# Kernel optimization log

Measured on AMD Instinct MI355X. Metric: run time of the kernel, lower is better.

Reference implementation:

```python
import jax, jax.numpy as jnp
import numpy as np

NUM_HEADS = 16
NUM_KV_HEADS = 4
HEAD_DIM = 128
LAYER_IDX = 5
MASK_VALUE = -65504.0  # torch.finfo(torch.float16).min


def setup_inputs() -> dict:
    key = jax.random.key(0)
    ks = jax.random.split(key, 7)
    B, S, H = 2, 2048, 2048
    hidden_states = jax.random.normal(ks[0], (B, S, H), dtype=jnp.float32)
    k = jax.random.normal(ks[1], (B, NUM_KV_HEADS, S, HEAD_DIM), dtype=jnp.float32)
    v = jax.random.normal(ks[2], (B, NUM_KV_HEADS, S, HEAD_DIM), dtype=jnp.float32)
    std = 0.02
    w_q = jax.random.normal(ks[3], (H, H), dtype=jnp.float32) * std
    b_q = jnp.zeros((H,), dtype=jnp.float32)
    w_proj = jax.random.normal(ks[4], (H, H), dtype=jnp.float32) * (std / np.sqrt(2 * 24))
    b_proj = jnp.zeros((H,), dtype=jnp.float32)
    return {"hidden_states": hidden_states, "key": k, "value": v,
            "w_q": w_q, "b_q": b_q, "w_proj": w_proj, "b_proj": b_proj}


def reference(hidden_states, key, value, w_q, b_q, w_proj, b_proj):
    B, S, H = hidden_states.shape
    G = NUM_HEADS // NUM_KV_HEADS  # query heads per kv head
    dtype = hidden_states.dtype

    # query projection -> [B, kv_heads, group, S, head_dim]
    q = hidden_states @ w_q.T + b_q
    q = q.reshape(B, S, NUM_KV_HEADS, G, HEAD_DIM).transpose(0, 2, 3, 1, 4)

    # bigcode-style fp32 softmax with layer-wise unscale
    unscale = float(LAYER_IDX + 1)  # scale_attention_softmax_in_fp32 and upcast
    scale_factor = (1.0 / unscale) * (HEAD_DIM ** -0.5)  # scale_attn_weights

    # scores: [B, kv_heads, group, S_q, S_k]
    scores = jnp.einsum('bkgsd,bktd->bkgst', q, key) * scale_factor

    causal = jnp.tril(jnp.ones((S, S), dtype=bool))  # [S_q, S_k]
    scores = jnp.where(causal, scores, jnp.asarray(MASK_VALUE, dtype=scores.dtype))

    probs = jax.nn.softmax((scores * unscale).astype(jnp.float32), axis=-1).astype(dtype)

    out = jnp.einsum('bkgst,bktd->bkgsd', probs, value)
    out = out.transpose(0, 3, 1, 2, 4).reshape(B, S, H)
    out = out @ w_proj.T + b_proj
    return out
```

## Files before the change

kernel.cpp:

```cpp
#include <hip/hip_runtime.h>
#include <math.h>


#define RSQ128 0.08838834764831845
#define LOG2E  1.4426950408889634
#define RS2L   ((float)(RSQ128 * LOG2E))
#define MASK2  (-567000.0f)
#define CAP2   24.0f

typedef __attribute__((ext_vector_type(8))) short short8;
typedef __attribute__((ext_vector_type(4))) float f32x4;
typedef __attribute__((ext_vector_type(16))) float f32x16;

static __device__ __forceinline__ unsigned short f2bf(float x) {
    union { float f; unsigned u; } v; v.f = x;
    unsigned r = v.u + 0x7FFFu + ((v.u >> 16) & 1u);
    return (unsigned short)(r >> 16);
}

static __device__ __forceinline__ unsigned pack_bf16(float lo, float hi) {
#if __has_builtin(__builtin_amdgcn_cvt_pk_bf16_f32)
    return __builtin_bit_cast(unsigned, __builtin_amdgcn_cvt_pk_bf16_f32(lo, hi));
#else
    return (unsigned)f2bf(lo) | ((unsigned)f2bf(hi) << 16);
#endif
}

static __device__ __forceinline__ float fexp2(float x) {
#if __has_builtin(__builtin_amdgcn_exp2f)
    return __builtin_amdgcn_exp2f(x);
#else
    return exp2f(x);
#endif
}

static __device__ __forceinline__ void gl_lds16(const void* g, void* l) {
    __builtin_amdgcn_global_load_lds(
        (const __attribute__((address_space(1))) void*)g,
        (__attribute__((address_space(3))) void*)l, 16, 0, 0);
}

__global__ void cvt_bf16(const float* __restrict__ in, unsigned short* __restrict__ out) {
    const int i = (blockIdx.x * 256 + threadIdx.x) * 8;
    const float4 a = *(const float4*)(in + i);
    const float4 b = *(const float4*)(in + i + 4);
    short8 o;
    o[0] = (short)f2bf(a.x); o[1] = (short)f2bf(a.y);
    o[2] = (short)f2bf(a.z); o[3] = (short)f2bf(a.w);
    o[4] = (short)f2bf(b.x); o[5] = (short)f2bf(b.y);
    o[6] = (short)f2bf(b.z); o[7] = (short)f2bf(b.w);
    *(short8*)(out + i) = o;
}

__global__ void kprep_bf16(const float* __restrict__ K, unsigned short* __restrict__ Kpk) {
    const int t = blockIdx.x, bkh = blockIdx.y, tid = threadIdx.x;
    const float* src = K + ((size_t)bkh * 2048 + t * 32) * 128;
    unsigned short* dst = Kpk + ((size_t)bkh * 64 + t) * 4096;
#pragma unroll
    for (int p = 0; p < 2; ++p) {
        const int g = p * 256 + tid;
        const int ch = g >> 5, key = g & 31;
        const float4 a = *(const float4*)(src + key * 128 + ch * 8);
        const float4 b = *(const float4*)(src + key * 128 + ch * 8 + 4);
        short8 o;
        o[0] = (short)f2bf(a.x); o[1] = (short)f2bf(a.y);
        o[2] = (short)f2bf(a.z); o[3] = (short)f2bf(a.w);
        o[4] = (short)f2bf(b.x); o[5] = (short)f2bf(b.y);
        o[6] = (short)f2bf(b.z); o[7] = (short)f2bf(b.w);
        *(short8*)(dst + ch * 256 + key * 8) = o;
    }
}

__global__ void vprep_bf16(const float* __restrict__ V, unsigned short* __restrict__ Vpk) {
    __shared__ float Ts[32][132];
    const int t = blockIdx.x, bkh = blockIdx.y, tid = threadIdx.x;
    const float* src = V + ((size_t)bkh * 2048 + t * 32) * 128;
    unsigned short* dst = Vpk + ((size_t)bkh * 64 + t) * 4096;
#pragma unroll
    for (int p = 0; p < 4; ++p) {
        const int g = p * 256 + tid;
        const int key = g >> 5, cq = g & 31;
        const float4 v = *(const float4*)(src + key * 128 + cq * 4);
        *(float4*)&Ts[key][cq * 4] = v;
    }
    __syncthreads();
#pragma unroll
    for (int p = 0; p < 2; ++p) {
        const int g = p * 256 + tid;
        const int kc = g >> 7, d = g & 127;
        short8 o;
#pragma unroll
        for (int j = 0; j < 8; ++j) o[j] = (short)f2bf(Ts[kc * 8 + j][d]);
        *(short8*)(dst + kc * 1024 + d * 8) = o;
    }
}

template <bool BF16OUT>
__global__ __launch_bounds__(512, 2) void gemm_nt_sk(
    const unsigned short* __restrict__ A,
    const unsigned short* __restrict__ W,
    const float* __restrict__ bias,
    void* __restrict__ Cout, int M, int N, int K, float oscale)
{
    __shared__ __align__(16) unsigned short SMEM[32768];
    unsigned short* Asb = SMEM;
    unsigned short* Wsb = SMEM + 16384;

    const int tid = threadIdx.x;
    const int g = tid >> 8;
    const int t2 = tid & 255;
    const int lane = tid & 63;
    const int wq = (tid >> 6) & 3;
    const int wm = wq & 1, wn = wq >> 1;
    const int m0 = blockIdx.y * 128, n0 = blockIdx.x * 128;
    const int r0 = t2 >> 2, c0 = t2 & 3;
    const int Kh = K >> 1;

    const unsigned short* Ag = A + (size_t)(m0 + r0) * K + g * Kh + c0 * 8;
    const unsigned short* Wg = W + (size_t)(n0 + r0) * K + g * Kh + c0 * 8;

    f32x4 acc[4][4];
#pragma unroll
    for (int i = 0; i < 4; ++i)
#pragma unroll
        for (int j = 0; j < 4; ++j) acc[i][j] = (f32x4){0.f, 0.f, 0.f, 0.f};

    const int lm = lane & 15, lk = (lane >> 4) * 8;
    unsigned short* As0 = Asb + g * 8192;
    unsigned short* Ws0 = Wsb + g * 8192;

    gl_lds16(Ag,                  As0 + t2 * 8);
    gl_lds16(Ag + (size_t)64 * K, As0 + (t2 + 256) * 8);
    gl_lds16(Wg,                  Ws0 + t2 * 8);
    gl_lds16(Wg + (size_t)64 * K, Ws0 + (t2 + 256) * 8);

    int buf = 0;
    for (int k0 = 0; k0 < Kh; k0 += 32) {
        __syncthreads();
        const int kn = k0 + 32;
        if (kn < Kh) {
            unsigned short* Ad = As0 + (buf ^ 1) * 4096;
            unsigned short* Wd = Ws0 + (buf ^ 1) * 4096;
            gl_lds16(Ag + kn,                  Ad + t2 * 8);
            gl_lds16(Ag + (size_t)64 * K + kn, Ad + (t2 + 256) * 8);
            gl_lds16(Wg + kn,                  Wd + t2 * 8);
            gl_lds16(Wg + (size_t)64 * K + kn, Wd + (t2 + 256) * 8);
        }

        const unsigned short* Ar = As0 + buf * 4096;
        const unsigned short* Wr = Ws0 + buf * 4096;
        short8 a[4], b[4];
#pragma unroll
        for (int i = 0; i < 4; ++i)
            a[i] = *(const short8*)&Ar[(64 * wm + 16 * i + lm) * 32 + lk];
#pragma unroll
        for (int j = 0; j < 4; ++j)
            b[j] = *(const short8*)&Wr[(64 * wn + 16 * j + lm) * 32 + lk];
#pragma unroll
        for (int i = 0; i < 4; ++i)
#pragma unroll
            for (int j = 0; j < 4; ++j)
                acc[i][j] = __builtin_amdgcn_mfma_f32_16x16x32_bf16(a[i], b[j], acc[i][j], 0, 0, 0);
        buf ^= 1;
    }

    float* MRG = (float*)SMEM;
    __syncthreads();
    if (g == 1) {
#pragma unroll
        for (int i = 0; i < 4; ++i)
#pragma unroll
            for (int j = 0; j < 4; ++j) {
                float4 v4;
                v4.x = acc[i][j][0]; v4.y = acc[i][j][1];
                v4.z = acc[i][j][2]; v4.w = acc[i][j][3];
                *(float4*)&MRG[((i * 4 + j) * 256 + wq * 64 + lane) * 4] = v4;
            }
    }
    __syncthreads();
    if (g == 0) {
        float bv[4];
#pragma unroll
        for (int j = 0; j < 4; ++j) bv[j] = bias[n0 + 64 * wn + 16 * j + lm];
#pragma unroll
        for (int i = 0; i < 4; ++i)
#pragma unroll
            for (int j = 0; j < 4; ++j) {
                const float4 v4 = *(const float4*)&MRG[((i * 4 + j) * 256 + wq * 64 + lane) * 4];
                const float s[4] = {v4.x, v4.y, v4.z, v4.w};
#pragma unroll
                for (int reg = 0; reg < 4; ++reg) {
                    const int row = m0 + 64 * wm + 16 * i + 4 * (lane >> 4) + reg;
                    const int col = n0 + 64 * wn + 16 * j + lm;
                    const float v = (acc[i][j][reg] + s[reg] + bv[j]) * oscale;
                    if (BF16OUT) ((unsigned short*)Cout)[(size_t)row * N + col] = f2bf(v);
                    else         ((float*)Cout)[(size_t)row * N + col] = v;
                }
            }
    }
}

__global__ __launch_bounds__(256, 4) void attn_mfma7(
    const unsigned short* __restrict__ Q,
    const unsigned short* __restrict__ Kpk,
    const unsigned short* __restrict__ Vpk,
    unsigned short* __restrict__ O)
{
    __shared__ __align__(16) unsigned short Ks[2][4096];
    __shared__ __align__(16) unsigned short Vs[2][4096];
    __shared__ float Lsm[2][64];

    const int tid = threadIdx.x, lane = tid & 63, w = tid >> 6;
    const int qhalf = w & 1, pz = w >> 1;
    const int h2 = lane >> 5, ln = lane & 31;

    const int bid = blockIdx.x;
    const int jj = bid >> 5;
    const int aa = jj & 7, bb = jj >> 3;
    const int qb = 8 * bb + ((bb & 1) ? (7 - aa) : aa);
    const int bh = bid & 31;
    const int s0 = qb * 64;
    const int b = bh >> 4, h = bh & 15, kh = h >> 2;

    const unsigned short* Kbase = Kpk + (size_t)(b * 4 + kh) * 64 * 4096;
    const unsigned short* Vbase = Vpk + (size_t)(b * 4 + kh) * 64 * 4096;

    const unsigned short* stsrc = (pz == 0 ? Kbase : Vbase) + (size_t)qhalf * 4096 + lane * 8;
    unsigned short* stdst = (pz == 0 ? Ks[qhalf] : Vs[qhalf]);

    const int qg = s0 + 32 * qhalf + ln;
    const unsigned short* Qp = Q + (size_t)(b * 2048 + qg) * 2048 + h * 128 + h2 * 8;
    short8 Qreg[8];
#pragma unroll
    for (int ks = 0; ks < 8; ++ks) Qreg[ks] = *(const short8*)(Qp + ks * 16);

    f32x16 Ot[4];
#pragma unroll
    for (int mt = 0; mt < 4; ++mt)
#pragma unroll
        for (int r = 0; r < 16; ++r) Ot[mt][r] = 0.f;
    float l_ = 0.f;

    const int wq_hi = s0 + 32 * qhalf + 31;
    const int myofs = 32 * pz;

    for (int j = 0; j <= qb; ++j) {
        __syncthreads();
        {
            const unsigned short* sp = stsrc + (size_t)j * 8192;
#pragma unroll
            for (int i = 0; i < 8; ++i)
                gl_lds16(sp + i * 512, stdst + i * 512);
        }
        __syncthreads();

        const int t0 = 64 * j + myofs;
        if (t0 <= wq_hi) {
            const unsigned short* KsA = Ks[pz] + h2 * 256 + ln * 8;
            const unsigned short* VsA = Vs[pz] + h2 * 1024 + ln * 8;

            f32x16 St;
#pragma unroll
            for (int r = 0; r < 16; ++r) St[r] = 0.f;
#pragma unroll
            for (int ks = 0; ks < 8; ++ks) {
                const short8 a = *(const short8*)(KsA + ks * 512);
                St = __builtin_amdgcn_mfma_f32_32x32x16_bf16(a, Qreg[ks], St, 0, 0, 0);
            }

            float s_loc = 0.f;
            unsigned Pp[8];
            if (t0 + 31 <= s0 + 32 * qhalf) {
#pragma unroll
                for (int p = 0; p < 8; ++p) {
                    const float p0 = fexp2(St[2 * p] - CAP2);
                    const float p1 = fexp2(St[2 * p + 1] - CAP2);
                    s_loc += p0 + p1;
                    Pp[p] = pack_bf16(p0, p1);
                }
            } else {
#pragma unroll
                for (int p = 0; p < 8; ++p) {
                    const int k0 = t0 + (2 * p & 3) + 8 * (2 * p >> 2) + 4 * h2;
                    const int k1 = t0 + ((2 * p + 1) & 3) + 8 * ((2 * p + 1) >> 2) + 4 * h2;
                    const float p0 = (k0 <= qg) ? fexp2(St[2 * p] - CAP2) : 0.f;
                    const float p1 = (k1 <= qg) ? fexp2(St[2 * p + 1] - CAP2) : 0.f;
                    s_loc += p0 + p1;
                    Pp[p] = pack_bf16(p0, p1);
                }
            }
            s_loc += __shfl_xor(s_loc, 32);
            l_ += s_loc;

#pragma unroll
            for (int ks4 = 0; ks4 < 2; ++ks4) {
                const unsigned pa = Pp[4 * ks4 + 0], pb = Pp[4 * ks4 + 1];
                const unsigned pc = Pp[4 * ks4 + 2], pd = Pp[4 * ks4 + 3];
                const unsigned x0 = (unsigned)__shfl_xor((int)(h2 ? pa : pc), 32);
                const unsigned x1 = (unsigned)__shfl_xor((int)(h2 ? pb : pd), 32);
                union { unsigned u[4]; short8 s8; } fr;
                fr.u[0] = h2 ? x0 : pa;
                fr.u[1] = h2 ? x1 : pb;
                fr.u[2] = h2 ? pc : x0;
                fr.u[3] = h2 ? pd : x1;
#pragma unroll
                for (int mt = 0; mt < 4; ++mt) {
                    const short8 a = *(const short8*)(VsA + ks4 * 2048 + mt * 256);
                    Ot[mt] = __builtin_amdgcn_mfma_f32_32x32x16_bf16(a, fr.s8, Ot[mt], 0, 0, 0);
                }
            }
        }
    }

    __syncthreads();
    if (pz == 1) {
        float* dst = qhalf ? (float*)Vs : (float*)Ks;
#pragma unroll
        for (int mt = 0; mt < 4; ++mt)
#pragma unroll
            for (int g = 0; g < 4; ++g) {
                float4 v4;
                v4.x = Ot[mt][4 * g + 0]; v4.y = Ot[mt][4 * g + 1];
                v4.z = Ot[mt][4 * g + 2]; v4.w = Ot[mt][4 * g + 3];
                *(float4*)&dst[lane * 64 + (((mt * 4 + g + lane) & 15) * 4)] = v4;
            }
        Lsm[qhalf][lane] = l_;
    }
    __syncthreads();
    if (pz == 0) {
        const float* src = qhalf ? (const float*)Vs : (const float*)Ks;
        l_ += Lsm[qhalf][lane];
#pragma unroll
        for (int mt = 0; mt < 4; ++mt)
#pragma unroll
            for (int g = 0; g < 4; ++g) {
                const float4 v4 = *(const float4*)&src[lane * 64 + (((mt * 4 + g + lane) & 15) * 4)];
                Ot[mt][4 * g + 0] += v4.x;
                Ot[mt][4 * g + 1] += v4.y;
                Ot[mt][4 * g + 2] += v4.z;
                Ot[mt][4 * g + 3] += v4.w;
            }
    }
    __syncthreads();

    if (pz == 0) {
        unsigned short* Es = (unsigned short*)Ks + qhalf * 4096;
        const float inv = 1.0f / l_;
#pragma unroll
        for (int mt = 0; mt < 4; ++mt)
#pragma unroll
            for (int g = 0; g < 4; ++g) {
                uint2 pk;
                pk.x = pack_bf16(Ot[mt][4 * g + 0] * inv, Ot[mt][4 * g + 1] * inv);
                pk.y = pack_bf16(Ot[mt][4 * g + 2] * inv, Ot[mt][4 * g + 3] * inv);
                const int chunk = (4 * mt + g) ^ (ln & 15);
                *(uint2*)&Es[ln * 128 + chunk * 8 + 4 * h2] = pk;
            }
    }
    __syncthreads();
    if (pz == 0) {
        unsigned short* Es = (unsigned short*)Ks + qhalf * 4096;
#pragma unroll
        for (int pp = 0; pp < 8; ++pp) {
            const int f = pp * 64 + lane;
            const int q = f >> 4, c = f & 15;
            const short8 v = *(const short8*)&Es[q * 128 + ((c ^ (q & 15)) * 8)];
            *(short8*)(O + (size_t)(b * 2048 + s0 + 32 * qhalf + q) * 2048 + h * 128 + c * 8) = v;
        }
    }
}

extern "C" void kernel_launch(void* const* d_in, const int* in_sizes, int n_in,
                              void* d_out, int out_size, void* d_ws, size_t ws_size,
                              hipStream_t stream) {
    const float* hs = (const float*)d_in[0];
    const float* k  = (const float*)d_in[1];
    const float* v  = (const float*)d_in[2];
    const float* wq = (const float*)d_in[3];
    const float* bq = (const float*)d_in[4];
    const float* wp = (const float*)d_in[5];
    const float* bp = (const float*)d_in[6];
    float* out = (float*)d_out;

    unsigned short* hsb  = (unsigned short*)d_ws;
    unsigned short* wqb  = hsb  + 8388608;
    unsigned short* kpk  = wqb  + 4194304;
    unsigned short* vpk  = kpk  + 2097152;
    unsigned short* qbuf = vpk  + 2097152;
    unsigned short* abuf = qbuf + 8388608;
    unsigned short* wpb  = hsb;

    cvt_bf16<<<4096, 256, 0, stream>>>(hs, hsb);
    cvt_bf16<<<2048, 256, 0, stream>>>(wq, wqb);
    kprep_bf16<<<dim3(64, 8), 256, 0, stream>>>(k, kpk);
    vprep_bf16<<<dim3(64, 8), 256, 0, stream>>>(v, vpk);

    dim3 gG(16, 32);
    gemm_nt_sk<true><<<gG, 512, 0, stream>>>(hsb, wqb, bq, qbuf, 4096, 2048, 2048, RS2L);
    cvt_bf16<<<2048, 256, 0, stream>>>(wp, wpb);
    attn_mfma7<<<1024, 256, 0, stream>>>(qbuf, kpk, vpk, abuf);
    gemm_nt_sk<false><<<gG, 512, 0, stream>>>(abuf, wpb, bp, out, 4096, 2048, 2048, 1.0f);
}
```

Measured before the change: 298.9 us.

## Pair causal query blocks per workgroup and double-buffer K/V LDS loads

The attention kernel now processes two query blocks per workgroup (qb and 31-qb), so each workgroup does an equal amount of causal work and the grid halves to 512 blocks. K/V tiles are double-buffered in LDS, with the next tile's global-to-LDS copy issued before computing on the current one and explicit vmcnt waits. Block indexing is reordered so neighbouring blocks share a kv head. LDS use doubles and launch bounds drop to 2 waves per EU, which lowers occupancy in exchange for overlapping loads with compute.

```diff
diff --git a/kernel.cpp b/kernel.cpp
--- a/kernel.cpp
+++ b/kernel.cpp
@@ -200,14 +200,14 @@
     }
 }
 
-__global__ __launch_bounds__(256, 4) void attn_mfma7(
+__global__ __launch_bounds__(256, 2) void attn_mfma8(
     const unsigned short* __restrict__ Q,
     const unsigned short* __restrict__ Kpk,
     const unsigned short* __restrict__ Vpk,
     unsigned short* __restrict__ O)
 {
-    __shared__ __align__(16) unsigned short Ks[2][4096];
-    __shared__ __align__(16) unsigned short Vs[2][4096];
+    __shared__ __align__(16) unsigned short Ks[2][2][4096];
+    __shared__ __align__(16) unsigned short Vs[2][2][4096];
     __shared__ float Lsm[2][64];
 
     const int tid = threadIdx.x, lane = tid & 63, w = tid >> 6;
@@ -215,157 +215,176 @@
     const int h2 = lane >> 5, ln = lane & 31;
 
     const int bid = blockIdx.x;
-    const int jj = bid >> 5;
-    const int aa = jj & 7, bb = jj >> 3;
-    const int qb = 8 * bb + ((bb & 1) ? (7 - aa) : aa);
-    const int bh = bid & 31;
-    const int s0 = qb * 64;
-    const int b = bh >> 4, h = bh & 15, kh = h >> 2;
+    const int grp = bid & 7;
+    const int idx = bid >> 3;
+    const int b = grp >> 2, kh = grp & 3;
+    const int pr = idx >> 2, hl = idx & 3;
+    const int h = kh * 4 + hl;
 
     const unsigned short* Kbase = Kpk + (size_t)(b * 4 + kh) * 64 * 4096;
     const unsigned short* Vbase = Vpk + (size_t)(b * 4 + kh) * 64 * 4096;
-
     const unsigned short* stsrc = (pz == 0 ? Kbase : Vbase) + (size_t)qhalf * 4096 + lane * 8;
-    unsigned short* stdst = (pz == 0 ? Ks[qhalf] : Vs[qhalf]);
-
-    const int qg = s0 + 32 * qhalf + ln;
-    const unsigned short* Qp = Q + (size_t)(b * 2048 + qg) * 2048 + h * 128 + h2 * 8;
-    short8 Qreg[8];
-#pragma unroll
-    for (int ks = 0; ks < 8; ++ks) Qreg[ks] = *(const short8*)(Qp + ks * 16);
-
-    f32x16 Ot[4];
-#pragma unroll
-    for (int mt = 0; mt < 4; ++mt)
-#pragma unroll
-        for (int r = 0; r < 16; ++r) Ot[mt][r] = 0.f;
-    float l_ = 0.f;
-
-    const int wq_hi = s0 + 32 * qhalf + 31;
     const int myofs = 32 * pz;
 
-    for (int j = 0; j <= qb; ++j) {
-        __syncthreads();
+    for (int ph = 0; ph < 2; ++ph) {
+        const int qb = ph ? pr : 31 - pr;
+        const int s0 = qb * 64;
+        const int qg = s0 + 32 * qhalf + ln;
+        const int wq_hi = s0 + 32 * qhalf + 31;
+
+        const unsigned short* Qp = Q + (size_t)(b * 2048 + qg) * 2048 + h * 128 + h2 * 8;
+        short8 Qreg[8];
+#pragma unroll
+        for (int ks = 0; ks < 8; ++ks) Qreg[ks] = *(const short8*)(Qp + ks * 16);
+
+        f32x16 Ot[4];
+#pragma unroll
+        for (int mt = 0; mt < 4; ++mt)
+#pragma unroll
+            for (int r = 0; r < 16; ++r) Ot[mt][r] = 0.f;
+        float l_ = 0.f;
+
+        __syncthreads();
+
         {
-            const unsigned short* sp = stsrc + (size_t)j * 8192;
+            unsigned short* sd = (pz == 0) ? &Ks[0][qhalf][0] : &Vs[0][qhalf][0];
 #pragma unroll
             for (int i = 0; i < 8; ++i)
-                gl_lds16(sp + i * 512, stdst + i * 512);
-        }
-        __syncthreads();
-
-        const int t0 = 64 * j + myofs;
-        if (t0 <= wq_hi) {
-            const unsigned short* KsA = Ks[pz] + h2 * 256 + ln * 8;
-            const unsigned short* VsA = Vs[pz] + h2 * 1024 + ln * 8;
-
-            f32x16 St;
-#pragma unroll
-            for (int r = 0; r < 16; ++r) St[r] = 0.f;
-#pragma unroll
-            for (int ks = 0; ks < 8; ++ks) {
-                const short8 a = *(const short8*)(KsA + ks * 512);
-                St = __builtin_amdgcn_mfma_f32_32x32x16_bf16(a, Qreg[ks], St, 0, 0, 0);
+                gl_lds16(stsrc + i * 512, sd + i * 512);
+        }
+
+        for (int j = 0; j <= qb; ++j) {
+            const int buf = j & 1;
+            if (j < qb) {
+                const unsigned short* sp = stsrc + (size_t)(j + 1) * 8192;
+                unsigned short* sd = (pz == 0) ? &Ks[buf ^ 1][qhalf][0] : &Vs[buf ^ 1][qhalf][0];
+#pragma unroll
+                for (int i = 0; i < 8; ++i)
+                    gl_lds16(sp + i * 512, sd + i * 512);
+                asm volatile("s_waitcnt vmcnt(8)" ::: "memory");
+            } else {
+                asm volatile("s_waitcnt vmcnt(0)" ::: "memory");
             }
-
-            float s_loc = 0.f;
-            unsigned Pp[8];
-            if (t0 + 31 <= s0 + 32 * qhalf) {
-#pragma unroll
-                for (int p = 0; p < 8; ++p) {
-                    const float p0 = fexp2(St[2 * p] - CAP2);
-                    const float p1 = fexp2(St[2 * p + 1] - CAP2);
-                    s_loc += p0 + p1;
-                    Pp[p] = pack_bf16(p0, p1);
-                }
-            } else {
-#pragma unroll
-                for (int p = 0; p < 8; ++p) {
-                    const int k0 = t0 + (2 * p & 3) + 8 * (2 * p >> 2) + 4 * h2;
-                    const int k1 = t0 + ((2 * p + 1) & 3) + 8 * ((2 * p + 1) >> 2) + 4 * h2;
-                    const float p0 = (k0 <= qg) ? fexp2(St[2 * p] - CAP2) : 0.f;
-                    const float p1 = (k1 <= qg) ? fexp2(St[2 * p + 1] - CAP2) : 0.f;
-                    s_loc += p0 + p1;
-                    Pp[p] = pack_bf16(p0, p1);
+            __builtin_amdgcn_s_barrier();
+            __builtin_amdgcn_sched_barrier(0);
+
+            const int t0 = 64 * j + myofs;
+            if (t0 <= wq_hi) {
+                const unsigned short* KsA = &Ks[buf][pz][0] + h2 * 256 + ln * 8;
+                const unsigned short* VsA = &Vs[buf][pz][0] + h2 * 1024 + ln * 8;
+
+                f32x16 St;
+#pragma unroll
+                for (int r = 0; r < 16; ++r) St[r] = 0.f;
+#pragma unroll
+                for (int ks = 0; ks < 8; ++ks) {
+                    const short8 a = *(const short8*)(KsA + ks * 512);
+                    St = __builtin_amdgcn_mfma_f32_32x32x16_bf16(a, Qreg[ks], St, 0, 0, 0);
+                }
+
+                float s_loc = 0.f;
+                unsigned Pp[8];
+                if (t0 + 31 <= s0 + 32 * qhalf) {
+#pragma unroll
+                    for (int p = 0; p < 8; ++p) {
+                        const float p0 = fexp2(St[2 * p] - CAP2);
+                        const float p1 = fexp2(St[2 * p + 1] - CAP2);
+                        s_loc += p0 + p1;
+                        Pp[p] = pack_bf16(p0, p1);
+                    }
+                } else {
+#pragma unroll
+                    for (int p = 0; p < 8; ++p) {
+                        const int k0 = t0 + (2 * p & 3) + 8 * (2 * p >> 2) + 4 * h2;
+                        const int k1 = t0 + ((2 * p + 1) & 3) + 8 * ((2 * p + 1) >> 2) + 4 * h2;
+                        const float p0 = (k0 <= qg) ? fexp2(St[2 * p] - CAP2) : 0.f;
+                        const float p1 = (k1 <= qg) ? fexp2(St[2 * p + 1] - CAP2) : 0.f;
+                        s_loc += p0 + p1;
+                        Pp[p] = pack_bf16(p0, p1);
+                    }
+                }
+                s_loc += __shfl_xor(s_loc, 32);
+                l_ += s_loc;
+
+#pragma unroll
+                for (int ks4 = 0; ks4 < 2; ++ks4) {
+                    const unsigned pa = Pp[4 * ks4 + 0], pb = Pp[4 * ks4 + 1];
+                    const unsigned pc = Pp[4 * ks4 + 2], pd = Pp[4 * ks4 + 3];
+                    const unsigned x0 = (unsigned)__shfl_xor((int)(h2 ? pa : pc), 32);
+                    const unsigned x1 = (unsigned)__shfl_xor((int)(h2 ? pb : pd), 32);
+                    union { unsigned u[4]; short8 s8; } fr;
+                    fr.u[0] = h2 ? x0 : pa;
+                    fr.u[1] = h2 ? x1 : pb;
+                    fr.u[2] = h2 ? pc : x0;
+                    fr.u[3] = h2 ? pd : x1;
+#pragma unroll
+                    for (int mt = 0; mt < 4; ++mt) {
+                        const short8 a = *(const short8*)(VsA + ks4 * 2048 + mt * 256);
+                        Ot[mt] = __builtin_amdgcn_mfma_f32_32x32x16_bf16(a, fr.s8, Ot[mt], 0, 0, 0);
+                    }
                 }
             }
-            s_loc += __shfl_xor(s_loc, 32);
-            l_ += s_loc;
-
-#pragma unroll
-            for (int ks4 = 0; ks4 < 2; ++ks4) {
-                const unsigned pa = Pp[4 * ks4 + 0], pb = Pp[4 * ks4 + 1];
-                const unsigned pc = Pp[4 * ks4 + 2], pd = Pp[4 * ks4 + 3];
-                const unsigned x0 = (unsigned)__shfl_xor((int)(h2 ? pa : pc), 32);
-                const unsigned x1 = (unsigned)__shfl_xor((int)(h2 ? pb : pd), 32);
-                union { unsigned u[4]; short8 s8; } fr;
-                fr.u[0] = h2 ? x0 : pa;
-                fr.u[1] = h2 ? x1 : pb;
-                fr.u[2] = h2 ? pc : x0;
-                fr.u[3] = h2 ? pd : x1;
-#pragma unroll
-                for (int mt = 0; mt < 4; ++mt) {
-                    const short8 a = *(const short8*)(VsA + ks4 * 2048 + mt * 256);
-                    Ot[mt] = __builtin_amdgcn_mfma_f32_32x32x16_bf16(a, fr.s8, Ot[mt], 0, 0, 0);
-                }
+
+            __builtin_amdgcn_sched_barrier(0);
+            __builtin_amdgcn_s_barrier();
+            __builtin_amdgcn_sched_barrier(0);
+        }
+
+        __syncthreads();
+        if (pz == 1) {
+            float* dst = qhalf ? (float*)Vs : (float*)Ks;
+#pragma unroll
+            for (int mt = 0; mt < 4; ++mt)
+#pragma unroll
+                for (int g = 0; g < 4; ++g) {
+                    float4 v4;
+                    v4.x = Ot[mt][4 * g + 0]; v4.y = Ot[mt][4 * g + 1];
+                    v4.z = Ot[mt][4 * g + 2]; v4.w = Ot[mt][4 * g + 3];
+                    *(float4*)&dst[lane * 64 + (((mt * 4 + g + lane) & 15) * 4)] = v4;
+                }
+            Lsm[qhalf][lane] = l_;
+        }
+        __syncthreads();
+        if (pz == 0) {
+            const float* src = qhalf ? (const float*)Vs : (const float*)Ks;
+            l_ += Lsm[qhalf][lane];
+#pragma unroll
+            for (int mt = 0; mt < 4; ++mt)
+#pragma unroll
+                for (int g = 0; g < 4; ++g) {
+                    const float4 v4 = *(const float4*)&src[lane * 64 + (((mt * 4 + g + lane) & 15) * 4)];
+                    Ot[mt][4 * g + 0] += v4.x;
+                    Ot[mt][4 * g + 1] += v4.y;
+                    Ot[mt][4 * g + 2] += v4.z;
+                    Ot[mt][4 * g + 3] += v4.w;
+                }
+        }
+        __syncthreads();
+
+        if (pz == 0) {
+            unsigned short* Es = (unsigned short*)Ks + qhalf * 4096;
+            const float inv = 1.0f / l_;
+#pragma unroll
+            for (int mt = 0; mt < 4; ++mt)
+#pragma unroll
+                for (int g = 0; g < 4; ++g) {
+                    uint2 pk;
+                    pk.x = pack_bf16(Ot[mt][4 * g + 0] * inv, Ot[mt][4 * g + 1] * inv);
+                    pk.y = pack_bf16(Ot[mt][4 * g + 2] * inv, Ot[mt][4 * g + 3] * inv);
+                    const int chunk = (4 * mt + g) ^ (ln & 15);
+                    *(uint2*)&Es[ln * 128 + chunk * 8 + 4 * h2] = pk;
+                }
+        }
+        __syncthreads();
+        if (pz == 0) {
+            unsigned short* Es = (unsigned short*)Ks + qhalf * 4096;
+#pragma unroll
+            for (int pp = 0; pp < 8; ++pp) {
+                const int f = pp * 64 + lane;
+                const int q = f >> 4, c = f & 15;
+                const short8 v = *(const short8*)&Es[q * 128 + ((c ^ (q & 15)) * 8)];
+                *(short8*)(O + (size_t)(b * 2048 + s0 + 32 * qhalf + q) * 2048 + h * 128 + c * 8) = v;
             }
-        }
-    }
-
-    __syncthreads();
-    if (pz == 1) {
-        float* dst = qhalf ? (float*)Vs : (float*)Ks;
-#pragma unroll
-        for (int mt = 0; mt < 4; ++mt)
-#pragma unroll
-            for (int g = 0; g < 4; ++g) {
-                float4 v4;
-                v4.x = Ot[mt][4 * g + 0]; v4.y = Ot[mt][4 * g + 1];
-                v4.z = Ot[mt][4 * g + 2]; v4.w = Ot[mt][4 * g + 3];
-                *(float4*)&dst[lane * 64 + (((mt * 4 + g + lane) & 15) * 4)] = v4;
-            }
-        Lsm[qhalf][lane] = l_;
-    }
-    __syncthreads();
-    if (pz == 0) {
-        const float* src = qhalf ? (const float*)Vs : (const float*)Ks;
-        l_ += Lsm[qhalf][lane];
-#pragma unroll
-        for (int mt = 0; mt < 4; ++mt)
-#pragma unroll
-            for (int g = 0; g < 4; ++g) {
-                const float4 v4 = *(const float4*)&src[lane * 64 + (((mt * 4 + g + lane) & 15) * 4)];
-                Ot[mt][4 * g + 0] += v4.x;
-                Ot[mt][4 * g + 1] += v4.y;
-                Ot[mt][4 * g + 2] += v4.z;
-                Ot[mt][4 * g + 3] += v4.w;
-            }
-    }
-    __syncthreads();
-
-    if (pz == 0) {
-        unsigned short* Es = (unsigned short*)Ks + qhalf * 4096;
-        const float inv = 1.0f / l_;
-#pragma unroll
-        for (int mt = 0; mt < 4; ++mt)
-#pragma unroll
-            for (int g = 0; g < 4; ++g) {
-                uint2 pk;
-                pk.x = pack_bf16(Ot[mt][4 * g + 0] * inv, Ot[mt][4 * g + 1] * inv);
-                pk.y = pack_bf16(Ot[mt][4 * g + 2] * inv, Ot[mt][4 * g + 3] * inv);
-                const int chunk = (4 * mt + g) ^ (ln & 15);
-                *(uint2*)&Es[ln * 128 + chunk * 8 + 4 * h2] = pk;
-            }
-    }
-    __syncthreads();
-    if (pz == 0) {
-        unsigned short* Es = (unsigned short*)Ks + qhalf * 4096;
-#pragma unroll
-        for (int pp = 0; pp < 8; ++pp) {
-            const int f = pp * 64 + lane;
-            const int q = f >> 4, c = f & 15;
-            const short8 v = *(const short8*)&Es[q * 128 + ((c ^ (q & 15)) * 8)];
-            *(short8*)(O + (size_t)(b * 2048 + s0 + 32 * qhalf + q) * 2048 + h * 128 + c * 8) = v;
         }
     }
 }
@@ -398,6 +417,6 @@
     dim3 gG(16, 32);
     gemm_nt_sk<true><<<gG, 512, 0, stream>>>(hsb, wqb, bq, qbuf, 4096, 2048, 2048, RS2L);
     cvt_bf16<<<2048, 256, 0, stream>>>(wp, wpb);
-    attn_mfma7<<<1024, 256, 0, stream>>>(qbuf, kpk, vpk, abuf);
+    attn_mfma8<<<512, 256, 0, stream>>>(qbuf, kpk, vpk, abuf);
     gemm_nt_sk<false><<<gG, 512, 0, stream>>>(abuf, wpb, bp, out, 4096, 2048, 2048, 1.0f);
 }
```

Result: faster. 273.6 us (-8.5%).

## Pair causal q-blocks per block and load K/V fragments directly into registers

Applied to the files above, without the earlier changes.

The attention kernel now launches 512 blocks, and each block handles two q-blocks (pr and 31-pr) in turn, which balances causal work across blocks. The LDS staging of K/V tiles and the per-iteration __syncthreads are removed. Each wave loads its K and V MFMA fragments straight from global memory into registers, relying on L2 reuse across the heads that share a KV head, which the new block ordering groups together. Launch bounds drop to 2 waves per EU to leave room for the larger register set. The risk is that global loads are no longer overlapped with compute and that occupancy is lower.

```diff
diff --git a/kernel.cpp b/kernel.cpp
--- a/kernel.cpp
+++ b/kernel.cpp
@@ -5,7 +5,6 @@
 #define RSQ128 0.08838834764831845
 #define LOG2E  1.4426950408889634
 #define RS2L   ((float)(RSQ128 * LOG2E))
-#define MASK2  (-567000.0f)
 #define CAP2   24.0f
 
 typedef __attribute__((ext_vector_type(8))) short short8;
@@ -200,14 +199,13 @@
     }
 }
 
-__global__ __launch_bounds__(256, 4) void attn_mfma7(
+__global__ __launch_bounds__(256, 2) void attn_mfma9(
     const unsigned short* __restrict__ Q,
     const unsigned short* __restrict__ Kpk,
     const unsigned short* __restrict__ Vpk,
     unsigned short* __restrict__ O)
 {
-    __shared__ __align__(16) unsigned short Ks[2][4096];
-    __shared__ __align__(16) unsigned short Vs[2][4096];
+    __shared__ __align__(16) float MRG[2][4096];
     __shared__ float Lsm[2][64];
 
     const int tid = threadIdx.x, lane = tid & 63, w = tid >> 6;
@@ -215,58 +213,59 @@
     const int h2 = lane >> 5, ln = lane & 31;
 
     const int bid = blockIdx.x;
-    const int jj = bid >> 5;
-    const int aa = jj & 7, bb = jj >> 3;
-    const int qb = 8 * bb + ((bb & 1) ? (7 - aa) : aa);
-    const int bh = bid & 31;
-    const int s0 = qb * 64;
-    const int b = bh >> 4, h = bh & 15, kh = h >> 2;
+    const int grp = bid & 7;
+    const int idx = bid >> 3;
+    const int b = grp >> 2, kh = grp & 3;
+    const int pr = idx >> 2, hl = idx & 3;
+    const int h = kh * 4 + hl;
 
     const unsigned short* Kbase = Kpk + (size_t)(b * 4 + kh) * 64 * 4096;
     const unsigned short* Vbase = Vpk + (size_t)(b * 4 + kh) * 64 * 4096;
-
-    const unsigned short* stsrc = (pz == 0 ? Kbase : Vbase) + (size_t)qhalf * 4096 + lane * 8;
-    unsigned short* stdst = (pz == 0 ? Ks[qhalf] : Vs[qhalf]);
-
-    const int qg = s0 + 32 * qhalf + ln;
-    const unsigned short* Qp = Q + (size_t)(b * 2048 + qg) * 2048 + h * 128 + h2 * 8;
-    short8 Qreg[8];
-#pragma unroll
-    for (int ks = 0; ks < 8; ++ks) Qreg[ks] = *(const short8*)(Qp + ks * 16);
-
-    f32x16 Ot[4];
-#pragma unroll
-    for (int mt = 0; mt < 4; ++mt)
-#pragma unroll
-        for (int r = 0; r < 16; ++r) Ot[mt][r] = 0.f;
-    float l_ = 0.f;
-
-    const int wq_hi = s0 + 32 * qhalf + 31;
+    const int koff = h2 * 256 + ln * 8;
+    const int voff = h2 * 1024 + ln * 8;
     const int myofs = 32 * pz;
 
-    for (int j = 0; j <= qb; ++j) {
-        __syncthreads();
-        {
-            const unsigned short* sp = stsrc + (size_t)j * 8192;
+    for (int ph = 0; ph < 2; ++ph) {
+        const int qb = ph ? pr : 31 - pr;
+        const int s0 = qb * 64;
+        const int qg = s0 + 32 * qhalf + ln;
+        const int wq_hi = s0 + 32 * qhalf + 31;
+
+        const unsigned short* Qp = Q + (size_t)(b * 2048 + qg) * 2048 + h * 128 + h2 * 8;
+        short8 Qreg[8];
+#pragma unroll
+        for (int ks = 0; ks < 8; ++ks) Qreg[ks] = *(const short8*)(Qp + ks * 16);
+
+        f32x16 Ot[4];
+#pragma unroll
+        for (int mt = 0; mt < 4; ++mt)
+#pragma unroll
+            for (int r = 0; r < 16; ++r) Ot[mt][r] = 0.f;
+        float l_ = 0.f;
+
+        __syncthreads();
+
+        for (int j = 0; j <= qb; ++j) {
+            const int t0 = 64 * j + myofs;
+            if (t0 > wq_hi) continue;
+
+            const unsigned short* Kt = Kbase + (size_t)(2 * j + pz) * 4096;
+            const unsigned short* Vt = Vbase + (size_t)(2 * j + pz) * 4096;
+
+            short8 kf[8], vf[8];
+#pragma unroll
+            for (int ks = 0; ks < 8; ++ks)
+                kf[ks] = *(const short8*)(Kt + ks * 512 + koff);
 #pragma unroll
             for (int i = 0; i < 8; ++i)
-                gl_lds16(sp + i * 512, stdst + i * 512);
-        }
-        __syncthreads();
-
-        const int t0 = 64 * j + myofs;
-        if (t0 <= wq_hi) {
-            const unsigned short* KsA = Ks[pz] + h2 * 256 + ln * 8;
-            const unsigned short* VsA = Vs[pz] + h2 * 1024 + ln * 8;
+                vf[i] = *(const short8*)(Vt + (i >> 2) * 2048 + (i & 3) * 256 + voff);
 
             f32x16 St;
 #pragma unroll
             for (int r = 0; r < 16; ++r) St[r] = 0.f;
 #pragma unroll
-            for (int ks = 0; ks < 8; ++ks) {
-                const short8 a = *(const short8*)(KsA + ks * 512);
-                St = __builtin_amdgcn_mfma_f32_32x32x16_bf16(a, Qreg[ks], St, 0, 0, 0);
-            }
+            for (int ks = 0; ks < 8; ++ks)
+                St = __builtin_amdgcn_mfma_f32_32x32x16_bf16(kf[ks], Qreg[ks], St, 0, 0, 0);
 
             float s_loc = 0.f;
             unsigned Pp[8];
@@ -304,68 +303,66 @@
                 fr.u[2] = h2 ? pc : x0;
                 fr.u[3] = h2 ? pd : x1;
 #pragma unroll
-                for (int mt = 0; mt < 4; ++mt) {
-                    const short8 a = *(const short8*)(VsA + ks4 * 2048 + mt * 256);
-                    Ot[mt] = __builtin_amdgcn_mfma_f32_32x32x16_bf16(a, fr.s8, Ot[mt], 0, 0, 0);
-                }
+                for (int mt = 0; mt < 4; ++mt)
+                    Ot[mt] = __builtin_amdgcn_mfma_f32_32x32x16_bf16(vf[ks4 * 4 + mt], fr.s8, Ot[mt], 0, 0, 0);
             }
         }
-    }
-
-    __syncthreads();
-    if (pz == 1) {
-        float* dst = qhalf ? (float*)Vs : (float*)Ks;
-#pragma unroll
-        for (int mt = 0; mt < 4; ++mt)
-#pragma unroll
-            for (int g = 0; g < 4; ++g) {
-                float4 v4;
-                v4.x = Ot[mt][4 * g + 0]; v4.y = Ot[mt][4 * g + 1];
-                v4.z = Ot[mt][4 * g + 2]; v4.w = Ot[mt][4 * g + 3];
-                *(float4*)&dst[lane * 64 + (((mt * 4 + g + lane) & 15) * 4)] = v4;
+
+        __syncthreads();
+        if (pz == 1) {
+            float* dst = MRG[qhalf];
+#pragma unroll
+            for (int mt = 0; mt < 4; ++mt)
+#pragma unroll
+                for (int g = 0; g < 4; ++g) {
+                    float4 v4;
+                    v4.x = Ot[mt][4 * g + 0]; v4.y = Ot[mt][4 * g + 1];
+                    v4.z = Ot[mt][4 * g + 2]; v4.w = Ot[mt][4 * g + 3];
+                    *(float4*)&dst[lane * 64 + (((mt * 4 + g + lane) & 15) * 4)] = v4;
+                }
+            Lsm[qhalf][lane] = l_;
+        }
+        __syncthreads();
+        if (pz == 0) {
+            const float* src = MRG[qhalf];
+            l_ += Lsm[qhalf][lane];
+#pragma unroll
+            for (int mt = 0; mt < 4; ++mt)
+#pragma unroll
+                for (int g = 0; g < 4; ++g) {
+                    const float4 v4 = *(const float4*)&src[lane * 64 + (((mt * 4 + g + lane) & 15) * 4)];
+                    Ot[mt][4 * g + 0] += v4.x;
+                    Ot[mt][4 * g + 1] += v4.y;
+                    Ot[mt][4 * g + 2] += v4.z;
+                    Ot[mt][4 * g + 3] += v4.w;
+                }
+        }
+        __syncthreads();
+
+        if (pz == 0) {
+            unsigned short* Es = (unsigned short*)MRG[qhalf];
+            const float inv = 1.0f / l_;
+#pragma unroll
+            for (int mt = 0; mt < 4; ++mt)
+#pragma unroll
+                for (int g = 0; g < 4; ++g) {
+                    uint2 pk;
+                    pk.x = pack_bf16(Ot[mt][4 * g + 0] * inv, Ot[mt][4 * g + 1] * inv);
+                    pk.y = pack_bf16(Ot[mt][4 * g + 2] * inv, Ot[mt][4 * g + 3] * inv);
+                    const int chunk = (4 * mt + g) ^ (ln & 15);
+                    *(uint2*)&Es[ln * 128 + chunk * 8 + 4 * h2] = pk;
+                }
+        }
+        __syncthreads();
+        if (pz == 0) {
+            unsigned short* Es = (unsigned short*)MRG[qhalf];
+#pragma unroll
+            for (int pp = 0; pp < 8; ++pp) {
+                const int f = pp * 64 + lane;
+                const int q = f >> 4, c = f & 15;
+                const short8 v = *(const short8*)&Es[q * 128 + ((c ^ (q & 15)) * 8)];
+                *(short8*)(O + (size_t)(b * 2048 + s0 + 32 * qhalf + q) * 2048 + h * 128 + c * 8) = v;
             }
-        Lsm[qhalf][lane] = l_;
-    }
-    __syncthreads();
-    if (pz == 0) {
-        const float* src = qhalf ? (const float*)Vs : (const float*)Ks;
-        l_ += Lsm[qhalf][lane];
-#pragma unroll
-        for (int mt = 0; mt < 4; ++mt)
-#pragma unroll
-            for (int g = 0; g < 4; ++g) {
-                const float4 v4 = *(const float4*)&src[lane * 64 + (((mt * 4 + g + lane) & 15) * 4)];
-                Ot[mt][4 * g + 0] += v4.x;
-                Ot[mt][4 * g + 1] += v4.y;
-                Ot[mt][4 * g + 2] += v4.z;
-                Ot[mt][4 * g + 3] += v4.w;
-            }
-    }
-    __syncthreads();
-
-    if (pz == 0) {
-        unsigned short* Es = (unsigned short*)Ks + qhalf * 4096;
-        const float inv = 1.0f / l_;
-#pragma unroll
-        for (int mt = 0; mt < 4; ++mt)
-#pragma unroll
-            for (int g = 0; g < 4; ++g) {
-                uint2 pk;
-                pk.x = pack_bf16(Ot[mt][4 * g + 0] * inv, Ot[mt][4 * g + 1] * inv);
-                pk.y = pack_bf16(Ot[mt][4 * g + 2] * inv, Ot[mt][4 * g + 3] * inv);
-                const int chunk = (4 * mt + g) ^ (ln & 15);
-                *(uint2*)&Es[ln * 128 + chunk * 8 + 4 * h2] = pk;
-            }
-    }
-    __syncthreads();
-    if (pz == 0) {
-        unsigned short* Es = (unsigned short*)Ks + qhalf * 4096;
-#pragma unroll
-        for (int pp = 0; pp < 8; ++pp) {
-            const int f = pp * 64 + lane;
-            const int q = f >> 4, c = f & 15;
-            const short8 v = *(const short8*)&Es[q * 128 + ((c ^ (q & 15)) * 8)];
-            *(short8*)(O + (size_t)(b * 2048 + s0 + 32 * qhalf + q) * 2048 + h * 128 + c * 8) = v;
         }
     }
 }
@@ -398,6 +395,6 @@
     dim3 gG(16, 32);
     gemm_nt_sk<true><<<gG, 512, 0, stream>>>(hsb, wqb, bq, qbuf, 4096, 2048, 2048, RS2L);
     cvt_bf16<<<2048, 256, 0, stream>>>(wp, wpb);
-    attn_mfma7<<<1024, 256, 0, stream>>>(qbuf, kpk, vpk, abuf);
+    attn_mfma9<<<512, 256, 0, stream>>>(qbuf, kpk, vpk, abuf);
     gemm_nt_sk<false><<<gG, 512, 0, stream>>>(abuf, wpb, bp, out, 4096, 2048, 2048, 1.0f);
 }
```

Result: faster. 284.8 us (-4.7%).
